# Kernel tuning notes

Hardware: AMD Instinct MI355X
Metric: run time of the kernel (lower is better)

Reference implementation:

```python
import jax, jax.numpy as jnp
import numpy as np

B, NQ, NK, D, DV = 16, 2048, 2048, 128, 128


def setup_inputs() -> dict:
    key = jax.random.key(0)
    kq, kk, kv, kl = jax.random.split(key, 4)
    return {
        "queries": jax.random.normal(kq, (B, NQ, D), dtype=jnp.float32),
        "keys": jax.random.normal(kk, (B, NK, D), dtype=jnp.float32),
        "values": jax.random.normal(kv, (B, NK, DV), dtype=jnp.float32),
        "valid_lens": jax.random.randint(kl, (B,), 1, NK + 1, dtype=jnp.int32),
    }


def reference(queries, keys, values, valid_lens):
    d = queries.shape[-1]
    # scores: [B, NQ, NK]
    scores = jnp.einsum("bqd,bkd->bqk", queries, keys) / jnp.sqrt(jnp.float32(d))
    # mask positions >= valid_len with -1e6 (matches sequence_mask semantics)
    key_pos = jnp.arange(scores.shape[-1], dtype=jnp.int32)  # [NK]
    mask = key_pos[None, None, :] < valid_lens[:, None, None]  # [B,1,NK] -> broadcast over queries
    scores = jnp.where(mask, scores, jnp.float32(-1000000.0))
    attn = jax.nn.softmax(scores, axis=-1)
    # dropout p=0.0 -> identity
    return jnp.einsum("bqk,bkv->bqv", attn, values)
```

## Files before the change

kernel.cpp:

```cpp
#include <hip/hip_runtime.h>


#define B_   16
#define NQ_  2048
#define NK_  2048
#define D_   128
#define DV_  128
#define NTASK_ 512

typedef unsigned short ushort;
typedef __attribute__((ext_vector_type(4))) float          f32x4;
typedef __attribute__((ext_vector_type(8))) __bf16         bf16x8;
typedef __attribute__((ext_vector_type(8))) unsigned short ushort8v;
typedef __attribute__((ext_vector_type(4))) unsigned int   uint4v;

#ifdef __has_builtin
#if __has_builtin(__builtin_amdgcn_cvt_pk_bf16_f32)
#define HAVE_CVT_PK_BF16 1
#endif
#endif

__device__ __forceinline__ ushort f2bf(float f) {
    unsigned u = __builtin_bit_cast(unsigned, f);
    return (ushort)((u + 0x8000u) >> 16);
}
__device__ __forceinline__ unsigned f2bf2(float a, float b) {
#ifdef HAVE_CVT_PK_BF16
    auto t = __builtin_amdgcn_cvt_pk_bf16_f32(a, b);
    return __builtin_bit_cast(unsigned, t);
#else
    return (unsigned)f2bf(a) | ((unsigned)f2bf(b) << 16);
#endif
}
__device__ __forceinline__ float bfpair_sum(unsigned u) {
    float lo = __builtin_bit_cast(float, u << 16);
    float hi = __builtin_bit_cast(float, u & 0xffff0000u);
    return lo + hi;
}
__device__ __forceinline__ void gl_lds16(const ushort* g, ushort* l) {
    __builtin_amdgcn_global_load_lds(
        (const __attribute__((address_space(1))) void*)g,
        (__attribute__((address_space(3))) void*)l, 16, 0, 0);
}

#define VL_STRIDE 132
__global__ __launch_bounds__(256) void convert_kv(
    const float* __restrict__ K, const float* __restrict__ V,
    const int* __restrict__ vlen, ushort* __restrict__ Kb, ushort* __restrict__ Vtb)
{
    __shared__ ushort Vl[64 * VL_STRIDE];
    const int id = blockIdx.x;
    const int b  = id & 15, kt = id >> 4;
    if (kt >= ((vlen[b] + 63) >> 6)) return;
    const int tid = threadIdx.x;
    const float* gK = K + ((size_t)b * NK_ + kt * 64) * D_;
    const float* gV = V + ((size_t)b * NK_ + kt * 64) * DV_;
    ushort* tK = Kb  + ((size_t)b * 32 + kt) * 8192;
    ushort* tV = Vtb + ((size_t)b * 32 + kt) * 8192;

    #pragma unroll
    for (int i = 0; i < 4; ++i) {
        int u = i * 256 + tid;
        int key = u >> 4, d8 = u & 15;
        const float* p = gK + key * D_ + d8 * 8;
        f32x4 a0 = *(const f32x4*)p;
        f32x4 a1 = *(const f32x4*)(p + 4);
        uint4v w;
        w[0] = f2bf2(a0[0], a0[1]); w[1] = f2bf2(a0[2], a0[3]);
        w[2] = f2bf2(a1[0], a1[1]); w[3] = f2bf2(a1[2], a1[3]);
        *(uint4v*)&tK[key * 128 + ((d8 ^ (key & 7)) << 3)] = w;
    }

    #pragma unroll
    for (int i = 0; i < 4; ++i) {
        int u = i * 256 + tid;
        int key = u >> 4, d8 = u & 15;
        const float* p = gV + key * DV_ + d8 * 8;
        f32x4 a0 = *(const f32x4*)p;
        f32x4 a1 = *(const f32x4*)(p + 4);
        uint4v w;
        w[0] = f2bf2(a0[0], a0[1]); w[1] = f2bf2(a0[2], a0[3]);
        w[2] = f2bf2(a1[0], a1[1]); w[3] = f2bf2(a1[2], a1[3]);
        *(uint4v*)&Vl[key * VL_STRIDE + d8 * 8] = w;
    }
    __syncthreads();

    #pragma unroll
    for (int i = 0; i < 4; ++i) {
        int u  = i * 256 + tid;
        int c  = u & 7, dv = u >> 3;
        int kg = c ^ (dv & 7);
        ushort v[8];
        #pragma unroll
        for (int j = 0; j < 8; ++j) v[j] = Vl[(kg * 8 + j) * VL_STRIDE + dv];
        uint4v w;
        w[0] = (unsigned)v[0] | ((unsigned)v[1] << 16);
        w[1] = (unsigned)v[2] | ((unsigned)v[3] << 16);
        w[2] = (unsigned)v[4] | ((unsigned)v[5] << 16);
        w[3] = (unsigned)v[6] | ((unsigned)v[7] << 16);
        *(uint4v*)&tV[dv * 64 + c * 8] = w;
    }
}

__global__ __launch_bounds__(512, 4) void attn_fwd(
    const float* __restrict__ Q, const int* __restrict__ vlen,
    const ushort* __restrict__ Kb, const ushort* __restrict__ Vtb,
    float* __restrict__ Out)
{
    __shared__ ushort KVbuf[2][16384];
    __shared__ float  lsh[2][64];
    __shared__ int    ssch[16];
    float* Osh = (float*)&KVbuf[0][0];

    const int tid  = threadIdx.x;
    const int w    = tid >> 6;
    const int wq   = w >> 1;
    const int wk   = w & 1;
    const int L    = tid & 63;
    const int col  = L & 15;
    const int quad = L >> 4;

    if (tid < 16) {
        int my = vlen[tid];
        int rank = 0;
        for (int o = 0; o < 16; ++o) {
            int vo = vlen[o];
            if (vo > my || (vo == my && o < tid)) ++rank;
        }
        ssch[rank] = tid;
    }
    __syncthreads();

    const int e     = blockIdx.x;
    const int p_    = (e & 255) >> 5;
    const int b     = (e >> 8) ? ssch[15 - p_] : ssch[p_];
    const int qbase = (e & 31) * 64;
    const int vl    = vlen[b];
    const int ntiles = (vl + 63) >> 6;

    const float qscale = 0.12751743f;
    bf16x8 qf[4];
    {
        const int qrow = qbase + wq * 16 + col;
        const float* gQ = Q + ((size_t)b * NQ_ + qrow) * D_;
        #pragma unroll
        for (int c = 0; c < 4; ++c) {
            const float* pp = gQ + c * 32 + quad * 8;
            f32x4 a0 = *(const f32x4*)pp;
            f32x4 a1 = *(const f32x4*)(pp + 4);
            uint4v us;
            us[0] = f2bf2(a0[0] * qscale, a0[1] * qscale);
            us[1] = f2bf2(a0[2] * qscale, a0[3] * qscale);
            us[2] = f2bf2(a1[0] * qscale, a1[1] * qscale);
            us[3] = f2bf2(a1[2] * qscale, a1[3] * qscale);
            qf[c] = __builtin_bit_cast(bf16x8, us);
        }
    }

    f32x4 o[8];
    #pragma unroll
    for (int d = 0; d < 8; ++d) o[d] = (f32x4){0.f, 0.f, 0.f, 0.f};
    float l_run = 0.f;

    const ushort* tKb = Kb  + (size_t)b * 32 * 8192;
    const ushort* tVb = Vtb + (size_t)b * 32 * 8192;

    #define ISSUE_DMA(KT, BUF)                                               \
        do {                                                                 \
            const ushort* gk = tKb + (size_t)(KT) * 8192;                    \
            const ushort* gv = tVb + (size_t)(KT) * 8192;                    \
            _Pragma("unroll")                                                \
            for (int i = 0; i < 2; ++i) {                                    \
                int off = (i * 512 + tid) * 8;                               \
                gl_lds16(gk + off, &KVbuf[BUF][off]);                        \
                gl_lds16(gv + off, &KVbuf[BUF][8192 + off]);                 \
            }                                                                \
        } while (0)

    ISSUE_DMA(0, 0);

    const int swz = col & 7;

    for (int kt = 0; kt < ntiles; ++kt) {
        const int buf = kt & 1;
        __syncthreads();
        if (kt + 1 < ntiles) ISSUE_DMA(kt + 1, buf ^ 1);

        const ushort* Kt = &KVbuf[buf][0];
        const ushort* Vt = &KVbuf[buf][8192];

        f32x4 s0 = (f32x4){0.f,0.f,0.f,0.f};
        f32x4 s1 = (f32x4){0.f,0.f,0.f,0.f};
        __builtin_amdgcn_s_setprio(1);
        {
            const int key0 = (wk * 32 + col) * 128;
            #pragma unroll
            for (int c = 0; c < 4; ++c) {
                bf16x8 kb = __builtin_bit_cast(bf16x8, *(const ushort8v*)
                    &Kt[key0 + (((c * 4 + quad) ^ swz) << 3)]);
                s0 = __builtin_amdgcn_mfma_f32_16x16x32_bf16(kb, qf[c], s0, 0, 0, 0);
            }
            #pragma unroll
            for (int c = 0; c < 4; ++c) {
                bf16x8 kb = __builtin_bit_cast(bf16x8, *(const ushort8v*)
                    &Kt[key0 + 16 * 128 + (((c * 4 + quad) ^ swz) << 3)]);
                s1 = __builtin_amdgcn_mfma_f32_16x16x32_bf16(kb, qf[c], s1, 0, 0, 0);
            }
        }
        __builtin_amdgcn_s_setprio(0);

        const int rem = vl - kt * 64 - wk * 32;
        if (rem < 32) {
            #pragma unroll
            for (int rr = 0; rr < 4; ++rr) {
                if (quad * 4 + rr >= rem)      s0[rr] = -1e30f;
                if (16 + quad * 4 + rr >= rem) s1[rr] = -1e30f;
            }
        }

        unsigned wA = f2bf2(exp2f(s0[0]), exp2f(s0[1]));
        unsigned wB = f2bf2(exp2f(s0[2]), exp2f(s0[3]));
        unsigned wC = f2bf2(exp2f(s1[0]), exp2f(s1[1]));
        unsigned wD = f2bf2(exp2f(s1[2]), exp2f(s1[3]));
        l_run += bfpair_sum(wA) + bfpair_sum(wB) + bfpair_sum(wC) + bfpair_sum(wD);

        asm("v_permlane32_swap_b32 %0, %1" : "+v"(wA), "+v"(wC));
        asm("v_permlane32_swap_b32 %0, %1" : "+v"(wB), "+v"(wD));
        asm("v_permlane16_swap_b32 %0, %1" : "+v"(wA), "+v"(wC));
        asm("v_permlane16_swap_b32 %0, %1" : "+v"(wB), "+v"(wD));
        uint4v pw;
        pw[0] = wA; pw[1] = wB; pw[2] = wC; pw[3] = wD;
        bf16x8 pa = __builtin_bit_cast(bf16x8, pw);

        __builtin_amdgcn_s_setprio(1);
        #pragma unroll
        for (int dvc = 0; dvc < 8; ++dvc) {
            const int dv = dvc * 16 + col;
            bf16x8 vb = __builtin_bit_cast(bf16x8, *(const ushort8v*)
                &Vt[dv * 64 + (((wk * 4 + quad) ^ swz) << 3)]);
            o[dvc] = __builtin_amdgcn_mfma_f32_16x16x32_bf16(pa, vb, o[dvc], 0, 0, 0);
        }
        __builtin_amdgcn_s_setprio(0);
    }
    #undef ISSUE_DMA

    l_run += __shfl_xor(l_run, 16, 64);
    l_run += __shfl_xor(l_run, 32, 64);

    __syncthreads();

    if (L < 16) lsh[wk][wq * 16 + L] = l_run;
    #pragma unroll
    for (int dvc = 0; dvc < 8; ++dvc)
        #pragma unroll
        for (int rr = 0; rr < 4; ++rr)
            Osh[wk * 8192 + (wq * 16 + quad * 4 + rr) * 128 + dvc * 16 + col]
                = o[dvc][rr];
    __syncthreads();

    float* gO = Out + ((size_t)b * NQ_ + qbase) * DV_;
    #pragma unroll
    for (int i = 0; i < 4; ++i) {
        int idx = i * 512 + tid;
        int row = idx >> 5;
        int dq  = idx & 31;
        f32x4 a0 = *(const f32x4*)&Osh[row * 128 + dq * 4];
        f32x4 a1 = *(const f32x4*)&Osh[8192 + row * 128 + dq * 4];
        float linv = 1.0f / (lsh[0][row] + lsh[1][row]);
        *(f32x4*)&gO[(size_t)row * DV_ + dq * 4] = (a0 + a1) * linv;
    }
}

extern "C" void kernel_launch(void* const* d_in, const int* in_sizes, int n_in,
                              void* d_out, int out_size, void* d_ws, size_t ws_size,
                              hipStream_t stream) {
    const float* Q  = (const float*)d_in[0];
    const float* K  = (const float*)d_in[1];
    const float* V  = (const float*)d_in[2];
    const int*   vl = (const int*)d_in[3];
    float* out = (float*)d_out;

    char* ws = (char*)d_ws;
    ushort* Kbuf = (ushort*)(ws + 4096);
    ushort* Vbuf = Kbuf + (size_t)B_ * 32 * 8192;

    convert_kv<<<dim3(512, 1, 1), dim3(256, 1, 1), 0, stream>>>(K, V, vl, Kbuf, Vbuf);
    attn_fwd<<<dim3(NTASK_, 1, 1), dim3(512, 1, 1), 0, stream>>>(
        Q, vl, Kbuf, Vbuf, out);
}
```

Baseline: 132.6 us.

## Split long key ranges across two blocks and combine partial outputs

Replaces the single-pass attention kernel with a split-K variant: for batches with more than 16 key tiles, two blocks each process half of the key tiles and write unnormalized partial outputs and row sums. A new combine kernel adds the halves and normalizes. The aim is to balance load across CUs when valid lengths vary widely. In exchange it costs an extra kernel launch, workspace traffic for partial results, and an extra pass over the output. The split is valid without max rescaling only because the kernel appears to use no running max.

```diff
diff --git a/kernel.cpp b/kernel.cpp
--- a/kernel.cpp
+++ b/kernel.cpp
@@ -6,7 +6,6 @@
 #define NK_  2048
 #define D_   128
 #define DV_  128
-#define NTASK_ 512
 
 typedef unsigned short ushort;
 typedef __attribute__((ext_vector_type(4))) float          f32x4;
@@ -102,9 +101,10 @@
     }
 }
 
-__global__ __launch_bounds__(512, 4) void attn_fwd(
+__global__ __launch_bounds__(512, 4) void attn_part(
     const float* __restrict__ Q, const int* __restrict__ vlen,
     const ushort* __restrict__ Kb, const ushort* __restrict__ Vtb,
+    float* __restrict__ wsO, float* __restrict__ wsl,
     float* __restrict__ Out)
 {
     __shared__ ushort KVbuf[2][16384];
@@ -131,12 +131,20 @@
     }
     __syncthreads();
 
-    const int e     = blockIdx.x;
-    const int p_    = (e & 255) >> 5;
-    const int b     = (e >> 8) ? ssch[15 - p_] : ssch[p_];
-    const int qbase = (e & 31) * 64;
-    const int vl    = vlen[b];
-    const int ntiles = (vl + 63) >> 6;
+    const int e       = blockIdx.x;
+    const int h       = e & 1;
+    const int task    = e >> 1;
+    const int r       = task & 15;
+    const int qt      = task >> 4;
+    const int b       = ssch[r];
+    const int qbase   = qt * 64;
+    const int vl      = vlen[b];
+    const int ntiles  = (vl + 63) >> 6;
+    const int split   = (ntiles > 16);
+    if (!split && h) return;
+    const int hh    = (ntiles + 1) >> 1;
+    const int kt_lo = (split && h) ? hh : 0;
+    const int kt_hi = split ? (h ? ntiles : hh) : ntiles;
 
     const float qscale = 0.12751743f;
     bf16x8 qf[4];
@@ -177,14 +185,14 @@
             }                                                                \
         } while (0)
 
-    ISSUE_DMA(0, 0);
+    ISSUE_DMA(kt_lo, 0);
 
     const int swz = col & 7;
 
-    for (int kt = 0; kt < ntiles; ++kt) {
-        const int buf = kt & 1;
+    for (int kt = kt_lo; kt < kt_hi; ++kt) {
+        const int buf = (kt - kt_lo) & 1;
         __syncthreads();
-        if (kt + 1 < ntiles) ISSUE_DMA(kt + 1, buf ^ 1);
+        if (kt + 1 < kt_hi) ISSUE_DMA(kt + 1, buf ^ 1);
 
         const ushort* Kt = &KVbuf[buf][0];
         const ushort* Vt = &KVbuf[buf][8192];
@@ -258,7 +266,9 @@
                 = o[dvc][rr];
     __syncthreads();
 
-    float* gO = Out + ((size_t)b * NQ_ + qbase) * DV_;
+    if (tid < 64) wsl[(size_t)task * 128 + h * 64 + tid] = lsh[0][tid] + lsh[1][tid];
+    float* dst = h ? (wsO + (size_t)task * 8192)
+                   : (Out + ((size_t)b * NQ_ + qbase) * DV_);
     #pragma unroll
     for (int i = 0; i < 4; ++i) {
         int idx = i * 512 + tid;
@@ -266,8 +276,50 @@
         int dq  = idx & 31;
         f32x4 a0 = *(const f32x4*)&Osh[row * 128 + dq * 4];
         f32x4 a1 = *(const f32x4*)&Osh[8192 + row * 128 + dq * 4];
-        float linv = 1.0f / (lsh[0][row] + lsh[1][row]);
-        *(f32x4*)&gO[(size_t)row * DV_ + dq * 4] = (a0 + a1) * linv;
+        *(f32x4*)&dst[(size_t)row * 128 + dq * 4] = a0 + a1;
+    }
+}
+
+__global__ __launch_bounds__(256) void combine_norm(
+    const int* __restrict__ vlen, const float* __restrict__ wsO,
+    const float* __restrict__ wsl, float* __restrict__ Out)
+{
+    __shared__ int ssch[16];
+    const int tid = threadIdx.x;
+    if (tid < 16) {
+        int my = vlen[tid];
+        int rank = 0;
+        for (int o = 0; o < 16; ++o) {
+            int vo = vlen[o];
+            if (vo > my || (vo == my && o < tid)) ++rank;
+        }
+        ssch[rank] = tid;
+    }
+    __syncthreads();
+
+    const int task  = blockIdx.x;
+    const int r     = task & 15;
+    const int qt    = task >> 4;
+    const int b     = ssch[r];
+    const int vl    = vlen[b];
+    const int split = (((vl + 63) >> 6) > 16);
+
+    float* gO = Out + ((size_t)b * NQ_ + (size_t)qt * 64) * DV_;
+    const float* pO = wsO + (size_t)task * 8192;
+    const float* pl = wsl + (size_t)task * 128;
+
+    #pragma unroll
+    for (int i = 0; i < 8; ++i) {
+        int idx = i * 256 + tid;
+        int row = idx >> 5;
+        int dq  = idx & 31;
+        f32x4 v = *(const f32x4*)&gO[(size_t)row * 128 + dq * 4];
+        float l = pl[row];
+        if (split) {
+            v += *(const f32x4*)&pO[(size_t)row * 128 + dq * 4];
+            l += pl[64 + row];
+        }
+        *(f32x4*)&gO[(size_t)row * 128 + dq * 4] = v * (1.0f / l);
     }
 }
 
@@ -281,10 +333,14 @@
     float* out = (float*)d_out;
 
     char* ws = (char*)d_ws;
-    ushort* Kbuf = (ushort*)(ws + 4096);
+    float*  wsl  = (float*)ws;
+    float*  wsO  = (float*)(ws + 256 * 1024);
+    ushort* Kbuf = (ushort*)(ws + 256 * 1024 + (size_t)512 * 8192 * 4);
     ushort* Vbuf = Kbuf + (size_t)B_ * 32 * 8192;
 
     convert_kv<<<dim3(512, 1, 1), dim3(256, 1, 1), 0, stream>>>(K, V, vl, Kbuf, Vbuf);
-    attn_fwd<<<dim3(NTASK_, 1, 1), dim3(512, 1, 1), 0, stream>>>(
-        Q, vl, Kbuf, Vbuf, out);
-}
+    attn_part<<<dim3(1024, 1, 1), dim3(512, 1, 1), 0, stream>>>(
+        Q, vl, Kbuf, Vbuf, wsO, wsl, out);
+    combine_norm<<<dim3(512, 1, 1), dim3(256, 1, 1), 0, stream>>>(
+        vl, wsO, wsl, out);
+}
```

Result: slower. 154.0 us (+16.2%).
